# Kernel optimization log

Hardware: AMD Instinct MI355X
Metric: run time of the kernel (lower is better)

## Reference

```python
import jax, jax.numpy as jnp
import numpy as np

N_NODES = 50000
N_EDGES = 800000
D_IN = 128
D_OUT = 128
NUM_RELS = 100


def setup_inputs() -> dict:
    key = jax.random.key(0)
    k1, k2, k3, k4, k5, k6, k7 = jax.random.split(key, 7)
    h = jax.random.normal(k1, (N_NODES, D_IN), dtype=jnp.float32)
    W = jax.random.normal(k2, (D_IN, D_OUT), dtype=jnp.float32) * 0.05
    attn = jax.random.normal(k3, (2 * D_OUT,), dtype=jnp.float32) * 0.05
    rel_emb = jax.random.normal(k4, (NUM_RELS, 1), dtype=jnp.float32)
    src = jax.random.randint(k5, (N_EDGES,), 0, N_NODES, dtype=jnp.int32)
    dst = jax.random.randint(k6, (N_EDGES,), 0, N_NODES, dtype=jnp.int32)
    etype = jax.random.randint(k7, (N_EDGES,), 0, NUM_RELS, dtype=jnp.int32)
    return {"h": h, "W": W, "attn": attn, "rel_emb": rel_emb,
            "src": src, "dst": dst, "etype": etype}


def reference(h, W, attn, rel_emb, src, dst, etype):
    # h: [N, d_in], W: [d_in, d_out], attn: [2*d_out], rel_emb: [R, 1]
    # src/dst/etype: [E]
    N = h.shape[0]
    d = W.shape[1]
    # padding_idx=0 in nn.Embedding -> row 0 is zero
    rel_table = rel_emb.at[0].set(0.0)
    z = h @ W  # [N, d_out]
    # attn_fc([z_src, z_dst]) = z_src @ a_l + z_dst @ a_r (split the concat-linear)
    s_src = z @ attn[:d]  # [N]
    s_dst = z @ attn[d:]  # [N]
    e = jax.nn.leaky_relu(s_src[src] + s_dst[dst])  # [E], slope 0.01 as in torch
    # segment softmax over incoming edges of each dst node
    m = jax.ops.segment_max(e, dst, num_segments=N)  # [N]
    ex = jnp.exp(e - m[dst])  # [E]
    denom = jax.ops.segment_sum(ex, dst, num_segments=N)  # [N]
    alpha = ex / denom[dst]  # [E]
    coef = rel_table[etype, 0] * alpha  # [E]  (rel_alpha * alpha)
    # weighted sum of source messages per destination node
    out = jax.ops.segment_sum(coef[:, None] * z[src], dst, num_segments=N)  # [N, d_out]
    return out
```

## Files before the change

### kernel.cpp

```cpp
#include <hip/hip_runtime.h>

#define D 128
#define GROWS 64
#define WIN 64
#define CAPW 1536
#define CBLK 256
#define CHUNK_MAX 3200
#define NWMAX 1024

typedef __attribute__((ext_vector_type(8))) short short8;
typedef __attribute__((ext_vector_type(4))) float float4v;

__device__ __forceinline__ ushort f2bf(float x) {
    uint u = __float_as_uint(x);
    return (ushort)((u + 0x7FFFu + ((u >> 16) & 1u)) >> 16);
}
__device__ __forceinline__ float bf_lo(uint u) { return __uint_as_float(u << 16); }
__device__ __forceinline__ float bf_hi(uint u) { return __uint_as_float(u & 0xFFFF0000u); }

__global__ __launch_bounds__(256) void convW_kernel(
    const float* __restrict__ W, ushort* __restrict__ Wtg, int* __restrict__ wincur)
{
    int idx = blockIdx.x * 256 + threadIdx.x;
    int k = idx >> 7, n = idx & 127;
    Wtg[n * 128 + k] = f2bf(W[idx]);
    if (idx < NWMAX) wincur[idx] = 0;
}

__global__ __launch_bounds__(512) void fusedA_kernel(
    const float* __restrict__ h, const ushort* __restrict__ Wtg,
    const float* __restrict__ attn,
    ushort* __restrict__ zb, float* __restrict__ s_src, float* __restrict__ s_dst,
    const int* __restrict__ src, const int* __restrict__ dst,
    const int* __restrict__ etype, int* __restrict__ wincur,
    uint* __restrict__ binned, int N, int E, int gblocks)
{
    __shared__ __align__(16) char smem[35616];
    const int tid = threadIdx.x;
    const int lane = tid & 63;
    const int wave = tid >> 6;

    if (blockIdx.x >= gblocks) {
        int* hist  = (int*)smem;
        int* loff  = (int*)(smem + 4096);
        int* cur   = (int*)(smem + 8192);
        int* gbase = (int*)(smem + 12288);
        int* wsum  = (int*)(smem + 16384);
        uint* pay  = (uint*)(smem + 16416);
        ushort* bid = (ushort*)(smem + 29216);

        hist[tid] = 0;
        hist[tid + 512] = 0;
        __syncthreads();

        const int cb = blockIdx.x - gblocks;
        const int cpb = (E + CBLK - 1) / CBLK;
        const int cs = cb * cpb;
        const int ce = min(cs + cpb, E);
        const int n = ce - cs;

        {
            int i = tid;
            for (; i + 1536 < n; i += 2048) {
                int d0 = dst[cs + i], d1 = dst[cs + i + 512];
                int d2 = dst[cs + i + 1024], d3 = dst[cs + i + 1536];
                atomicAdd(&hist[d0 >> 6], 1);
                atomicAdd(&hist[d1 >> 6], 1);
                atomicAdd(&hist[d2 >> 6], 1);
                atomicAdd(&hist[d3 >> 6], 1);
            }
            for (; i < n; i += 512) atomicAdd(&hist[dst[cs + i] >> 6], 1);
        }
        __syncthreads();

        {
            int v0 = hist[2 * tid];
            int v1 = hist[2 * tid + 1];
            int s = v0 + v1;
            int incl = s;
#pragma unroll
            for (int off = 1; off < 64; off <<= 1) {
                int u = __shfl_up(incl, off);
                if (lane >= off) incl += u;
            }
            if (lane == 63) wsum[wave] = incl;
            __syncthreads();
            int woff = 0;
#pragma unroll
            for (int w = 0; w < 8; ++w)
                if (w < wave) woff += wsum[w];
            incl += woff;
            int e0 = incl - s;
            int e1 = e0 + v0;
            loff[2 * tid] = e0;
            loff[2 * tid + 1] = e1;
            cur[2 * tid] = e0;
            cur[2 * tid + 1] = e1;
            if (v0 > 0) gbase[2 * tid] = atomicAdd(&wincur[2 * tid], v0);
            if (v1 > 0) gbase[2 * tid + 1] = atomicAdd(&wincur[2 * tid + 1], v1);
        }
        __syncthreads();

        for (int i = tid; i < n; i += 512) {
            int dd = dst[cs + i];
            int b = dd >> 6;
            uint pk = (uint)src[cs + i] | ((uint)etype[cs + i] << 16) | ((uint)(dd & 63) << 23);
            int pos = atomicAdd(&cur[b], 1);
            if (pos < CHUNK_MAX) { pay[pos] = pk; bid[pos] = (ushort)b; }
        }
        __syncthreads();

        for (int i = tid; i < n; i += 512) {
            int b = bid[i];
            int local = gbase[b] + (i - loff[b]);
            if (local < CAPW) binned[(size_t)b * CAPW + local] = pay[i];
        }
        return;
    }

    ushort* ht = (ushort*)smem;
    float (*psum_s)[2] = (float(*)[2])(smem + 17408);
    float (*psum_d)[2] = (float(*)[2])(smem + 17920);
    const int base = blockIdx.x * GROWS;

#pragma unroll
    for (int it = 0; it < 4; ++it) {
        int idx = it * 512 + tid;
        int r = idx >> 5, c4 = (idx & 31) * 4;
        float4 v = make_float4(0.f, 0.f, 0.f, 0.f);
        if (base + r < N) v = *(const float4*)&h[(size_t)(base + r) * D + c4];
        ushort4 u = make_ushort4(f2bf(v.x), f2bf(v.y), f2bf(v.z), f2bf(v.w));
        *(ushort4*)&ht[r * 136 + c4] = u;
    }
    __syncthreads();

    const int wr = wave >> 1;
    const int wc = wave & 1;
    const int col = lane & 15;
    const int quad = lane >> 4;
    const int wm = wr * 16;

    float4v acc[4];
#pragma unroll
    for (int nt = 0; nt < 4; ++nt) acc[nt] = (float4v)(0.f);

#pragma unroll
    for (int kc = 0; kc < 128; kc += 32) {
        short8 a = *(const short8*)&ht[(wm + col) * 136 + kc + quad * 8];
#pragma unroll
        for (int nt = 0; nt < 4; ++nt) {
            short8 b = *(const short8*)&Wtg[(wc * 64 + nt * 16 + col) * 128 + kc + quad * 8];
            acc[nt] = __builtin_amdgcn_mfma_f32_16x16x32_bf16(a, b, acc[nt], 0, 0, 0);
        }
    }
    __syncthreads();

    float ps[4] = {0.f, 0.f, 0.f, 0.f}, pd[4] = {0.f, 0.f, 0.f, 0.f};
#pragma unroll
    for (int nt = 0; nt < 4; ++nt) {
        float aL = attn[wc * 64 + nt * 16 + col];
        float aR = attn[D + wc * 64 + nt * 16 + col];
#pragma unroll
        for (int reg = 0; reg < 4; ++reg) {
            float v = acc[nt][reg];
            ps[reg] = fmaf(v, aL, ps[reg]);
            pd[reg] = fmaf(v, aR, pd[reg]);
            ht[(wm + quad * 4 + reg) * 136 + wc * 64 + nt * 16 + col] = f2bf(v);
        }
    }
#pragma unroll
    for (int reg = 0; reg < 4; ++reg) {
#pragma unroll
        for (int off = 1; off < 16; off <<= 1) {
            ps[reg] += __shfl_xor(ps[reg], off);
            pd[reg] += __shfl_xor(pd[reg], off);
        }
        if (col == 0) {
            int rl = wm + quad * 4 + reg;
            psum_s[rl][wc] = ps[reg];
            psum_d[rl][wc] = pd[reg];
        }
    }
    __syncthreads();

    if (tid < GROWS && base + tid < N) {
        s_src[base + tid] = psum_s[tid][0] + psum_s[tid][1];
        s_dst[base + tid] = psum_d[tid][0] + psum_d[tid][1];
    }

#pragma unroll
    for (int it = 0; it < 2; ++it) {
        int idx = it * 512 + tid;
        int r = idx >> 4, c8 = idx & 15;
        if (base + r < N)
            *(uint4*)&zb[(size_t)(base + r) * D + c8 * 8] = *(uint4*)&ht[r * 136 + c8 * 8];
    }
}

__global__ __launch_bounds__(512) void fusedB_kernel(
    const uint* __restrict__ binned, const int* __restrict__ wincur,
    const float* __restrict__ s_src, const float* __restrict__ s_dst,
    const float* __restrict__ rel_emb, const uint* __restrict__ zb32,
    float* __restrict__ out, int N, int R)
{
    __shared__ float rel_l[128];
    __shared__ int hist[WIN];
    __shared__ int loff[WIN + 1];
    __shared__ int cur[WIN];
    __shared__ float sDst[WIN];
    __shared__ float sDen[WIN];
    __shared__ uint2 sS[CAPW];
    const int tid = threadIdx.x;
    const int lane = tid & 63;
    const int wave = tid >> 6;
    const int w = blockIdx.x;
    const int dbase = w * WIN;

    if (tid < R) rel_l[tid] = (tid == 0) ? 0.f : rel_emb[tid];
    if (tid < WIN) {
        hist[tid] = 0;
        sDen[tid] = 0.f;
        int dd = dbase + tid;
        sDst[tid] = (dd < N) ? s_dst[dd] : 0.f;
    }
    const int ne = min(wincur[w], CAPW);
    const uint* bbp = binned + (size_t)w * CAPW;

    uint pks[3];
#pragma unroll
    for (int j = 0; j < 3; ++j) {
        int i = tid + j * 512;
        pks[j] = (i < ne) ? bbp[i] : 0u;
    }
    __syncthreads();

#pragma unroll
    for (int j = 0; j < 3; ++j) {
        int i = tid + j * 512;
        if (i < ne) atomicAdd(&hist[(pks[j] >> 23) & 63], 1);
    }
    __syncthreads();

    if (wave == 0) {
        int hc = hist[lane];
        int incl = hc;
#pragma unroll
        for (int off = 1; off < 64; off <<= 1) {
            int u = __shfl_up(incl, off);
            if (lane >= off) incl += u;
        }
        loff[lane + 1] = incl;
        if (lane == 0) loff[0] = 0;
        cur[lane] = incl - hc;
    }
    __syncthreads();

#pragma unroll
    for (int j = 0; j < 3; ++j) {
        int i = tid + j * 512;
        if (i < ne) {
            uint pk = pks[j];
            int li = (int)((pk >> 23) & 63);
            int et = (int)((pk >> 16) & 0x7F);
            float x = s_src[pk & 0xFFFF] + sDst[li];
            float e = (x > 0.f) ? x : 0.01f * x;
            float p = __expf(e);
            int pos = atomicAdd(&cur[li], 1);
            if (pos < CAPW) sS[pos] = make_uint2(pk & 0xFFFF, __float_as_uint(p * rel_l[et]));
            atomicAdd(&sDen[li], p);
        }
    }
    __syncthreads();

    const int q = lane >> 4;
    const int ql = lane & 15;
    const int qid = wave * 4 + q;

    for (int nIdx = qid; nIdx < WIN; nIdx += 32) {
        const int d = dbase + nIdx;
        if (d >= N) continue;
        const int st = min(loff[nIdx], CAPW);
        const int en = min(loff[nIdx + 1], CAPW);
        const float den = sDen[nIdx];
        const float inv = (den > 0.f) ? 1.0f / den : 0.f;

        float4 acc0 = make_float4(0.f, 0.f, 0.f, 0.f);
        float4 acc1 = make_float4(0.f, 0.f, 0.f, 0.f);

        for (int b2 = st; b2 < en; b2 += 8) {
            uint2 hdr[8];
#pragma unroll
            for (int j = 0; j < 8; ++j) {
                int idx = b2 + j;
                hdr[j] = (idx < en) ? sS[idx] : make_uint2(0u, 0u);
            }
            uint4 u[8];
#pragma unroll
            for (int j = 0; j < 8; ++j)
                u[j] = *(const uint4*)(zb32 + (size_t)hdr[j].x * 64 + ql * 4);
#pragma unroll
            for (int j = 0; j < 8; ++j) {
                const float wj = __uint_as_float(hdr[j].y);
                acc0.x = fmaf(wj, bf_lo(u[j].x), acc0.x);
                acc0.y = fmaf(wj, bf_hi(u[j].x), acc0.y);
                acc0.z = fmaf(wj, bf_lo(u[j].y), acc0.z);
                acc0.w = fmaf(wj, bf_hi(u[j].y), acc0.w);
                acc1.x = fmaf(wj, bf_lo(u[j].z), acc1.x);
                acc1.y = fmaf(wj, bf_hi(u[j].z), acc1.y);
                acc1.z = fmaf(wj, bf_lo(u[j].w), acc1.z);
                acc1.w = fmaf(wj, bf_hi(u[j].w), acc1.w);
            }
        }

        float* orow = out + (size_t)d * D + ql * 8;
        *(float4*)orow       = make_float4(acc0.x * inv, acc0.y * inv, acc0.z * inv, acc0.w * inv);
        *(float4*)(orow + 4) = make_float4(acc1.x * inv, acc1.y * inv, acc1.z * inv, acc1.w * inv);
    }
}

extern "C" void kernel_launch(void* const* d_in, const int* in_sizes, int n_in,
                              void* d_out, int out_size, void* d_ws, size_t ws_size,
                              hipStream_t stream)
{
    const float* h    = (const float*)d_in[0];
    const float* W    = (const float*)d_in[1];
    const float* attn = (const float*)d_in[2];
    const float* rel  = (const float*)d_in[3];
    const int*   src  = (const int*)d_in[4];
    const int*   dst  = (const int*)d_in[5];
    const int*   et   = (const int*)d_in[6];
    float* out = (float*)d_out;

    const int N = in_sizes[0] / D;
    const int E = in_sizes[4];
    const int R = in_sizes[3];

    char* p = (char*)d_ws;
    auto alloc = [&](size_t bytes) {
        char* q = p;
        p += (bytes + 255) & ~(size_t)255;
        return q;
    };
    const int NW      = (N + WIN - 1) / WIN;
    const int gblocks = (N + GROWS - 1) / GROWS;

    ushort* zb     = (ushort*)alloc((size_t)N * D * sizeof(ushort));
    ushort* Wtg    = (ushort*)alloc((size_t)D * D * sizeof(ushort));
    float* ssrc    = (float*)alloc((size_t)N * sizeof(float));
    float* sdst    = (float*)alloc((size_t)N * sizeof(float));
    uint*  binned  = (uint*)alloc((size_t)NW * CAPW * sizeof(uint));
    int*   wincur  = (int*)alloc(NWMAX * sizeof(int));

    convW_kernel<<<64, 256, 0, stream>>>(W, Wtg, wincur);
    fusedA_kernel<<<gblocks + CBLK, 512, 0, stream>>>(h, Wtg, attn, zb, ssrc, sdst,
                                                      src, dst, et, wincur, binned,
                                                      N, E, gblocks);
    fusedB_kernel<<<NW, 512, 0, stream>>>(binned, wincur, ssrc, sdst, rel,
                                          (const uint*)zb, out, N, R);
}
```

Baseline: 151.7 us.

## Fold W conversion into fused GEMM blocks and prefetch gather headers

Removes the separate W-conversion kernel. Each GEMM block now loads fp32 W, converts it to bf16 and stores it transposed in padded LDS, and a memset replaces the counter zeroing that kernel used to do. In the aggregation loop, the next batch of edge headers is read from LDS while the current zb row gathers are in flight, overlapping the LDS and global latencies. The cost is redundant W conversion in every GEMM block and more LDS per block (about 52 KB), which may lower occupancy of fusedA.

```diff
diff --git a/kernel.cpp b/kernel.cpp
--- a/kernel.cpp
+++ b/kernel.cpp
@@ -18,24 +18,15 @@
 __device__ __forceinline__ float bf_lo(uint u) { return __uint_as_float(u << 16); }
 __device__ __forceinline__ float bf_hi(uint u) { return __uint_as_float(u & 0xFFFF0000u); }
 
-__global__ __launch_bounds__(256) void convW_kernel(
-    const float* __restrict__ W, ushort* __restrict__ Wtg, int* __restrict__ wincur)
-{
-    int idx = blockIdx.x * 256 + threadIdx.x;
-    int k = idx >> 7, n = idx & 127;
-    Wtg[n * 128 + k] = f2bf(W[idx]);
-    if (idx < NWMAX) wincur[idx] = 0;
-}
-
 __global__ __launch_bounds__(512) void fusedA_kernel(
-    const float* __restrict__ h, const ushort* __restrict__ Wtg,
+    const float* __restrict__ h, const float* __restrict__ W,
     const float* __restrict__ attn,
     ushort* __restrict__ zb, float* __restrict__ s_src, float* __restrict__ s_dst,
     const int* __restrict__ src, const int* __restrict__ dst,
     const int* __restrict__ etype, int* __restrict__ wincur,
     uint* __restrict__ binned, int N, int E, int gblocks)
 {
-    __shared__ __align__(16) char smem[35616];
+    __shared__ __align__(16) char smem[53248];
     const int tid = threadIdx.x;
     const int lane = tid & 63;
     const int wave = tid >> 6;
@@ -119,10 +110,23 @@
     }
 
     ushort* ht = (ushort*)smem;
-    float (*psum_s)[2] = (float(*)[2])(smem + 17408);
-    float (*psum_d)[2] = (float(*)[2])(smem + 17920);
+    ushort* wt = (ushort*)(smem + 17408);
+    float (*psum_s)[2] = (float(*)[2])(smem + 52224);
+    float (*psum_d)[2] = (float(*)[2])(smem + 52736);
     const int base = blockIdx.x * GROWS;
 
+#pragma unroll
+    for (int it = 0; it < 8; ++it) {
+        int idx = it * 512 + tid;
+        int nn = idx & 127;
+        int k4 = (idx >> 7) * 4;
+        float a0 = W[(k4 + 0) * 128 + nn];
+        float a1 = W[(k4 + 1) * 128 + nn];
+        float a2 = W[(k4 + 2) * 128 + nn];
+        float a3 = W[(k4 + 3) * 128 + nn];
+        ushort4 u = make_ushort4(f2bf(a0), f2bf(a1), f2bf(a2), f2bf(a3));
+        *(ushort4*)&wt[nn * 136 + k4] = u;
+    }
 #pragma unroll
     for (int it = 0; it < 4; ++it) {
         int idx = it * 512 + tid;
@@ -149,7 +153,7 @@
         short8 a = *(const short8*)&ht[(wm + col) * 136 + kc + quad * 8];
 #pragma unroll
         for (int nt = 0; nt < 4; ++nt) {
-            short8 b = *(const short8*)&Wtg[(wc * 64 + nt * 16 + col) * 128 + kc + quad * 8];
+            short8 b = *(const short8*)&wt[(wc * 64 + nt * 16 + col) * 136 + kc + quad * 8];
             acc[nt] = __builtin_amdgcn_mfma_f32_16x16x32_bf16(a, b, acc[nt], 0, 0, 0);
         }
     }
@@ -287,28 +291,38 @@
         float4 acc0 = make_float4(0.f, 0.f, 0.f, 0.f);
         float4 acc1 = make_float4(0.f, 0.f, 0.f, 0.f);
 
-        for (int b2 = st; b2 < en; b2 += 8) {
-            uint2 hdr[8];
+        if (en > st) {
+            uint2 hdr[8], hdrn[8];
 #pragma unroll
             for (int j = 0; j < 8; ++j) {
-                int idx = b2 + j;
+                int idx = st + j;
                 hdr[j] = (idx < en) ? sS[idx] : make_uint2(0u, 0u);
             }
-            uint4 u[8];
-#pragma unroll
-            for (int j = 0; j < 8; ++j)
-                u[j] = *(const uint4*)(zb32 + (size_t)hdr[j].x * 64 + ql * 4);
-#pragma unroll
-            for (int j = 0; j < 8; ++j) {
-                const float wj = __uint_as_float(hdr[j].y);
-                acc0.x = fmaf(wj, bf_lo(u[j].x), acc0.x);
-                acc0.y = fmaf(wj, bf_hi(u[j].x), acc0.y);
-                acc0.z = fmaf(wj, bf_lo(u[j].y), acc0.z);
-                acc0.w = fmaf(wj, bf_hi(u[j].y), acc0.w);
-                acc1.x = fmaf(wj, bf_lo(u[j].z), acc1.x);
-                acc1.y = fmaf(wj, bf_hi(u[j].z), acc1.y);
-                acc1.z = fmaf(wj, bf_lo(u[j].w), acc1.z);
-                acc1.w = fmaf(wj, bf_hi(u[j].w), acc1.w);
+            for (int b2 = st; b2 < en; b2 += 8) {
+                uint4 u[8];
+#pragma unroll
+                for (int j = 0; j < 8; ++j)
+                    u[j] = *(const uint4*)(zb32 + (size_t)hdr[j].x * 64 + ql * 4);
+                const int nb = b2 + 8;
+#pragma unroll
+                for (int j = 0; j < 8; ++j) {
+                    int idx = nb + j;
+                    hdrn[j] = (idx < en) ? sS[idx] : make_uint2(0u, 0u);
+                }
+#pragma unroll
+                for (int j = 0; j < 8; ++j) {
+                    const float wj = __uint_as_float(hdr[j].y);
+                    acc0.x = fmaf(wj, bf_lo(u[j].x), acc0.x);
+                    acc0.y = fmaf(wj, bf_hi(u[j].x), acc0.y);
+                    acc0.z = fmaf(wj, bf_lo(u[j].y), acc0.z);
+                    acc0.w = fmaf(wj, bf_hi(u[j].y), acc0.w);
+                    acc1.x = fmaf(wj, bf_lo(u[j].z), acc1.x);
+                    acc1.y = fmaf(wj, bf_hi(u[j].z), acc1.y);
+                    acc1.z = fmaf(wj, bf_lo(u[j].w), acc1.z);
+                    acc1.w = fmaf(wj, bf_hi(u[j].w), acc1.w);
+                }
+#pragma unroll
+                for (int j = 0; j < 8; ++j) hdr[j] = hdrn[j];
             }
         }
 
@@ -345,14 +359,13 @@
     const int gblocks = (N + GROWS - 1) / GROWS;
 
     ushort* zb     = (ushort*)alloc((size_t)N * D * sizeof(ushort));
-    ushort* Wtg    = (ushort*)alloc((size_t)D * D * sizeof(ushort));
     float* ssrc    = (float*)alloc((size_t)N * sizeof(float));
     float* sdst    = (float*)alloc((size_t)N * sizeof(float));
     uint*  binned  = (uint*)alloc((size_t)NW * CAPW * sizeof(uint));
     int*   wincur  = (int*)alloc(NWMAX * sizeof(int));
 
-    convW_kernel<<<64, 256, 0, stream>>>(W, Wtg, wincur);
-    fusedA_kernel<<<gblocks + CBLK, 512, 0, stream>>>(h, Wtg, attn, zb, ssrc, sdst,
+    hipMemsetAsync(wincur, 0, NWMAX * sizeof(int), stream);
+    fusedA_kernel<<<gblocks + CBLK, 512, 0, stream>>>(h, W, attn, zb, ssrc, sdst,
                                                       src, dst, et, wincur, binned,
                                                       N, E, gblocks);
     fusedB_kernel<<<NW, 512, 0, stream>>>(binned, wincur, ssrc, sdst, rel,
```

Result: faster. 147.0 us (-3.1%).

## Scatter binned edges directly, launch binning blocks first, prefetch gather headers

Applied to the files above, without the earlier changes.

The binning path drops its per-block prefix scan and shared-memory staging, so each edge is written straight to global memory at its window base plus a local atomic slot. Binning blocks now take the first block indices so they get scheduled ahead of the GEMM blocks, and shared memory is cut to 18 KB with a launch-bounds hint so more blocks fit per CU. The aggregation loop in the second kernel software-prefetches the next eight edge headers from LDS while the current gathers are in flight. In exchange, global writes within a bin are no longer contiguous runs, and edge order inside a bin becomes nondeterministic, which can change float summation order.

```diff
diff --git a/kernel.cpp b/kernel.cpp
--- a/kernel.cpp
+++ b/kernel.cpp
@@ -5,7 +5,6 @@
 #define WIN 64
 #define CAPW 1536
 #define CBLK 256
-#define CHUNK_MAX 3200
 #define NWMAX 1024
 
 typedef __attribute__((ext_vector_type(8))) short short8;
@@ -27,7 +26,7 @@
     if (idx < NWMAX) wincur[idx] = 0;
 }
 
-__global__ __launch_bounds__(512) void fusedA_kernel(
+__global__ __launch_bounds__(512, 8) void fusedA_kernel(
     const float* __restrict__ h, const ushort* __restrict__ Wtg,
     const float* __restrict__ attn,
     ushort* __restrict__ zb, float* __restrict__ s_src, float* __restrict__ s_dst,
@@ -35,25 +34,21 @@
     const int* __restrict__ etype, int* __restrict__ wincur,
     uint* __restrict__ binned, int N, int E, int gblocks)
 {
-    __shared__ __align__(16) char smem[35616];
+    __shared__ __align__(16) char smem[18432];
     const int tid = threadIdx.x;
     const int lane = tid & 63;
     const int wave = tid >> 6;
 
-    if (blockIdx.x >= gblocks) {
+    if (blockIdx.x < CBLK) {
         int* hist  = (int*)smem;
-        int* loff  = (int*)(smem + 4096);
-        int* cur   = (int*)(smem + 8192);
-        int* gbase = (int*)(smem + 12288);
-        int* wsum  = (int*)(smem + 16384);
-        uint* pay  = (uint*)(smem + 16416);
-        ushort* bid = (ushort*)(smem + 29216);
+        int* cur   = (int*)(smem + 4096);
+        int* gbase = (int*)(smem + 8192);
 
         hist[tid] = 0;
         hist[tid + 512] = 0;
         __syncthreads();
 
-        const int cb = blockIdx.x - gblocks;
+        const int cb = blockIdx.x;
         const int cpb = (E + CBLK - 1) / CBLK;
         const int cs = cb * cpb;
         const int ce = min(cs + cpb, E);
@@ -74,30 +69,12 @@
         __syncthreads();
 
         {
-            int v0 = hist[2 * tid];
-            int v1 = hist[2 * tid + 1];
-            int s = v0 + v1;
-            int incl = s;
-#pragma unroll
-            for (int off = 1; off < 64; off <<= 1) {
-                int u = __shfl_up(incl, off);
-                if (lane >= off) incl += u;
-            }
-            if (lane == 63) wsum[wave] = incl;
-            __syncthreads();
-            int woff = 0;
-#pragma unroll
-            for (int w = 0; w < 8; ++w)
-                if (w < wave) woff += wsum[w];
-            incl += woff;
-            int e0 = incl - s;
-            int e1 = e0 + v0;
-            loff[2 * tid] = e0;
-            loff[2 * tid + 1] = e1;
-            cur[2 * tid] = e0;
-            cur[2 * tid + 1] = e1;
-            if (v0 > 0) gbase[2 * tid] = atomicAdd(&wincur[2 * tid], v0);
-            if (v1 > 0) gbase[2 * tid + 1] = atomicAdd(&wincur[2 * tid + 1], v1);
+            int e0 = 2 * tid, e1 = 2 * tid + 1;
+            int v0 = hist[e0], v1 = hist[e1];
+            if (v0 > 0) gbase[e0] = atomicAdd(&wincur[e0], v0);
+            if (v1 > 0) gbase[e1] = atomicAdd(&wincur[e1], v1);
+            cur[e0] = 0;
+            cur[e1] = 0;
         }
         __syncthreads();
 
@@ -106,14 +83,8 @@
             int b = dd >> 6;
             uint pk = (uint)src[cs + i] | ((uint)etype[cs + i] << 16) | ((uint)(dd & 63) << 23);
             int pos = atomicAdd(&cur[b], 1);
-            if (pos < CHUNK_MAX) { pay[pos] = pk; bid[pos] = (ushort)b; }
-        }
-        __syncthreads();
-
-        for (int i = tid; i < n; i += 512) {
-            int b = bid[i];
-            int local = gbase[b] + (i - loff[b]);
-            if (local < CAPW) binned[(size_t)b * CAPW + local] = pay[i];
+            int local = gbase[b] + pos;
+            if (local < CAPW) binned[(size_t)b * CAPW + local] = pk;
         }
         return;
     }
@@ -121,7 +92,7 @@
     ushort* ht = (ushort*)smem;
     float (*psum_s)[2] = (float(*)[2])(smem + 17408);
     float (*psum_d)[2] = (float(*)[2])(smem + 17920);
-    const int base = blockIdx.x * GROWS;
+    const int base = (blockIdx.x - CBLK) * GROWS;
 
 #pragma unroll
     for (int it = 0; it < 4; ++it) {
@@ -287,28 +258,38 @@
         float4 acc0 = make_float4(0.f, 0.f, 0.f, 0.f);
         float4 acc1 = make_float4(0.f, 0.f, 0.f, 0.f);
 
-        for (int b2 = st; b2 < en; b2 += 8) {
-            uint2 hdr[8];
+        if (en > st) {
+            uint2 hdr[8], hdrn[8];
 #pragma unroll
             for (int j = 0; j < 8; ++j) {
-                int idx = b2 + j;
+                int idx = st + j;
                 hdr[j] = (idx < en) ? sS[idx] : make_uint2(0u, 0u);
             }
-            uint4 u[8];
-#pragma unroll
-            for (int j = 0; j < 8; ++j)
-                u[j] = *(const uint4*)(zb32 + (size_t)hdr[j].x * 64 + ql * 4);
-#pragma unroll
-            for (int j = 0; j < 8; ++j) {
-                const float wj = __uint_as_float(hdr[j].y);
-                acc0.x = fmaf(wj, bf_lo(u[j].x), acc0.x);
-                acc0.y = fmaf(wj, bf_hi(u[j].x), acc0.y);
-                acc0.z = fmaf(wj, bf_lo(u[j].y), acc0.z);
-                acc0.w = fmaf(wj, bf_hi(u[j].y), acc0.w);
-                acc1.x = fmaf(wj, bf_lo(u[j].z), acc1.x);
-                acc1.y = fmaf(wj, bf_hi(u[j].z), acc1.y);
-                acc1.z = fmaf(wj, bf_lo(u[j].w), acc1.z);
-                acc1.w = fmaf(wj, bf_hi(u[j].w), acc1.w);
+            for (int b2 = st; b2 < en; b2 += 8) {
+                uint4 u[8];
+#pragma unroll
+                for (int j = 0; j < 8; ++j)
+                    u[j] = *(const uint4*)(zb32 + (size_t)hdr[j].x * 64 + ql * 4);
+                const int nb = b2 + 8;
+#pragma unroll
+                for (int j = 0; j < 8; ++j) {
+                    int idx = nb + j;
+                    hdrn[j] = (idx < en) ? sS[idx] : make_uint2(0u, 0u);
+                }
+#pragma unroll
+                for (int j = 0; j < 8; ++j) {
+                    const float wj = __uint_as_float(hdr[j].y);
+                    acc0.x = fmaf(wj, bf_lo(u[j].x), acc0.x);
+                    acc0.y = fmaf(wj, bf_hi(u[j].x), acc0.y);
+                    acc0.z = fmaf(wj, bf_lo(u[j].y), acc0.z);
+                    acc0.w = fmaf(wj, bf_hi(u[j].y), acc0.w);
+                    acc1.x = fmaf(wj, bf_lo(u[j].z), acc1.x);
+                    acc1.y = fmaf(wj, bf_hi(u[j].z), acc1.y);
+                    acc1.z = fmaf(wj, bf_lo(u[j].w), acc1.z);
+                    acc1.w = fmaf(wj, bf_hi(u[j].w), acc1.w);
+                }
+#pragma unroll
+                for (int j = 0; j < 8; ++j) hdr[j] = hdrn[j];
             }
         }
 
@@ -352,7 +333,7 @@
     int*   wincur  = (int*)alloc(NWMAX * sizeof(int));
 
     convW_kernel<<<64, 256, 0, stream>>>(W, Wtg, wincur);
-    fusedA_kernel<<<gblocks + CBLK, 512, 0, stream>>>(h, Wtg, attn, zb, ssrc, sdst,
+    fusedA_kernel<<<CBLK + gblocks, 512, 0, stream>>>(h, Wtg, attn, zb, ssrc, sdst,
                                                       src, dst, et, wincur, binned,
                                                       N, E, gblocks);
     fusedB_kernel<<<NW, 512, 0, stream>>>(binned, wincur, ssrc, sdst, rel,
```

Result: slower. 155.2 us (+2.3%).
